# Performance work log

Measured on AMD Instinct MI355X. Metric: run time of the kernel, lower is better.

## Reference

```python
import jax, jax.numpy as jnp
import numpy as np

L, S, M, N, E, H = 1024, 1024, 256, 8, 512, 8


def embed_rotary(x, cos, sin):
    # x: [B, T, E]; interleaved rotate-half as in RotaryPositionEncoding.embed_rotary
    x2 = jnp.stack([-x[..., 1::2], x[..., 0::2]], axis=-1).reshape(x.shape)
    return x * cos + x2 * sin


def setup_inputs() -> dict:
    key = jax.random.key(0)
    ks = jax.random.split(key, 12)
    return {
        "query": jax.random.normal(ks[0], (L, N, E), jnp.float32),
        "key": jax.random.normal(ks[1], (S, N, E), jnp.float32),
        "value": jax.random.normal(ks[2], (S, N, E), jnp.float32),
        "in_proj_weight": jax.random.normal(ks[3], (3 * E, E), jnp.float32) / np.sqrt(E).astype(np.float32),
        "in_proj_bias": jnp.zeros((3 * E,), jnp.float32),
        "out_proj_weight": jax.random.normal(ks[4], (E, E), jnp.float32) / np.sqrt(E).astype(np.float32),
        "out_proj_bias": jnp.zeros((E,), jnp.float32),
        "rot_q": jax.random.normal(ks[5], (N, L, E, 2), jnp.float32),
        "rot_k": jax.random.normal(ks[6], (N, S, E, 2), jnp.float32),
        "k_mem": jax.random.normal(ks[7], (M, N, E), jnp.float32),
        "v_mem": jax.random.normal(ks[8], (M, N, E), jnp.float32),
        "gate_attn": jax.random.normal(ks[9], (H,), jnp.float32),
        "mem_mask": jax.random.randint(ks[10], (N, M), 0, 2).astype(bool),
        "num_heads": H,
    }


def reference(query, key, value, in_proj_weight, in_proj_bias, out_proj_weight,
              out_proj_bias, rot_q, rot_k, k_mem, v_mem, gate_attn, mem_mask, num_heads):
    L_, N_, E_ = query.shape
    S_ = key.shape[0]
    H_ = num_heads
    hd = E_ // H_
    scale = float(hd) ** -0.5
    # separate q/k/v projections (qkv not identical path)
    q = query @ in_proj_weight[:E_].T + in_proj_bias[:E_]
    k = key @ in_proj_weight[E_:2 * E_].T + in_proj_bias[E_:2 * E_]
    v = value @ in_proj_weight[2 * E_:].T + in_proj_bias[2 * E_:]
    q = q * scale
    # inline rotary PE (applied in batch-first layout, then back)
    q = embed_rotary(q.transpose(1, 0, 2), rot_q[..., 0], rot_q[..., 1]).transpose(1, 0, 2)
    k = embed_rotary(k.transpose(1, 0, 2), rot_k[..., 0], rot_k[..., 1]).transpose(1, 0, 2)
    qh = q.reshape(L_, N_, H_, hd).transpose(1, 2, 0, 3)  # [N,H,L,hd]
    kh = k.reshape(S_, N_, H_, hd).transpose(1, 2, 0, 3)  # [N,H,S,hd]
    vh = v.reshape(S_, N_, H_, hd).transpose(1, 2, 0, 3)
    scores = jnp.einsum('nhld,nhsd->nhls', qh, kh)
    # slot-competition: softmax over queries (slots), then renormalize over keys
    w = jax.nn.softmax(scores, axis=2) + 1e-8
    w = w / w.sum(axis=-1, keepdims=True)
    attn = jnp.einsum('nhls,nhsd->nhld', w, vh)
    # memorizing-transformer style memory K/V branch with sigmoid head gating
    Mm = k_mem.shape[0]
    km = k_mem.reshape(Mm, N_, H_, hd).transpose(1, 2, 0, 3)  # [N,H,M,hd]
    vm = v_mem.reshape(Mm, N_, H_, hd).transpose(1, 2, 0, 3)
    sm = jnp.einsum('nhld,nhmd->nhlm', qh, km)
    sm = jnp.where(mem_mask[:, None, None, :], -1e9, sm)  # additive -inf mask
    wm = jax.nn.softmax(sm, axis=-1)
    om = jnp.einsum('nhlm,nhmd->nhld', wm, vm)
    gate = jax.nn.sigmoid(gate_attn)[None, :, None, None]  # [1,H,1,1]
    attn = gate * om + (1.0 - gate) * attn
    out = attn.transpose(2, 0, 1, 3).reshape(L_, N_, E_)  # back to [L,N,E]
    return out @ out_proj_weight.T + out_proj_bias
```

## Files before the change

### kernel.cpp

```cpp
#include <hip/hip_runtime.h>
#include <hip/hip_bf16.h>

typedef __hip_bfloat16 bf16;
typedef __bf16 bf16x8 __attribute__((ext_vector_type(8)));
typedef float f32x4 __attribute__((ext_vector_type(4)));

#define LQ 1024
#define SK 1024
#define MMEM 256
#define NB 8
#define EE 512
#define NH 8
#define HD 64
#define NBH 64

__device__ inline __bf16 tobf(float f) {
  __hip_bfloat16 h = __float2bfloat16(f);
  return *reinterpret_cast<__bf16*>(&h);
}
__device__ inline float bf2f(__bf16 x) {
  unsigned short u; __builtin_memcpy(&u, &x, 2);
  unsigned int v = (unsigned int)u << 16;
  float f; __builtin_memcpy(&f, &v, 4);
  return f;
}
__device__ inline f32x4 MFMA(bf16x8 a, bf16x8 b, f32x4 c) {
  return __builtin_amdgcn_mfma_f32_16x16x32_bf16(a, b, c, 0, 0, 0);
}

__device__ inline bf16x8 load8(const float* p) {
  float4 a = *(const float4*)p;
  float4 b = *(const float4*)(p + 4);
  bf16x8 r;
  r[0] = tobf(a.x); r[1] = tobf(a.y); r[2] = tobf(a.z); r[3] = tobf(a.w);
  r[4] = tobf(b.x); r[5] = tobf(b.y); r[6] = tobf(b.z); r[7] = tobf(b.w);
  return r;
}

#define CVT_T0 524288
#define CVT_T3 98304
#define CVT_T4 32768
__global__ __launch_bounds__(256) void convert5(
    const float* __restrict__ q, const float* __restrict__ k,
    const float* __restrict__ v, const float* __restrict__ w,
    const float* __restrict__ o, bf16* __restrict__ qc, bf16* __restrict__ kc,
    bf16* __restrict__ vc, bf16* __restrict__ wc, bf16* __restrict__ oc)
{
  long long t = (long long)blockIdx.x * 256 + threadIdx.x;
  const float* src; bf16* dst; long long idx;
  if (t < CVT_T0)               { src = q; dst = qc; idx = t; }
  else if (t < 2 * CVT_T0)      { src = k; dst = kc; idx = t - CVT_T0; }
  else if (t < 3 * CVT_T0)      { src = v; dst = vc; idx = t - 2 * CVT_T0; }
  else if (t < 3 * CVT_T0 + CVT_T3) { src = w; dst = wc; idx = t - 3 * CVT_T0; }
  else                          { src = o; dst = oc; idx = t - 3 * CVT_T0 - CVT_T3; }
  *(bf16x8*)(dst + idx * 8) = load8(src + idx * 8);
}

__global__ __launch_bounds__(256) void gemm_proj3(
    const bf16* __restrict__ qc, const bf16* __restrict__ kc,
    const bf16* __restrict__ vc, const bf16* __restrict__ ipwb,
    const float* __restrict__ ipb, const float* __restrict__ rot_q,
    const float* __restrict__ rot_k, bf16* __restrict__ Qh,
    bf16* __restrict__ Kh, bf16* __restrict__ v_raw)
{
  __shared__ __align__(16) char smem[25600];
  __bf16 (*As)[40] = (__bf16(*)[40])smem;
  __bf16 (*Bs)[40] = (__bf16(*)[40])(smem + 5120);
  __bf16 (*Cs)[72] = (__bf16(*)[72])smem;
  const int z = blockIdx.z;
  const bf16* A = (z == 0) ? qc : (z == 1) ? kc : vc;
  const bf16* W = ipwb + (long long)z * EE * EE;
  const float* bias = ipb + z * EE;
  const float alpha = (z == 0) ? 0.125f : 1.f;
  const int tm0 = blockIdx.y << 6, tn0 = blockIdx.x << 8;
  const int t = threadIdx.x;
  const int lrow = t >> 2, lk = (t & 3) << 3;
  const int wave = t >> 6, lane = t & 63;
  const int wm = (wave & 1) << 5, wn = (wave >> 1) << 5;
  const int m16 = lane & 15, quad = lane >> 4;

  const f32x4 zero = {0.f, 0.f, 0.f, 0.f};
  f32x4 acc[4][2][2];
#pragma unroll
  for (int g = 0; g < 4; ++g)
#pragma unroll
    for (int mi = 0; mi < 2; ++mi)
#pragma unroll
      for (int ni = 0; ni < 2; ++ni) acc[g][mi][ni] = zero;

  const bf16* ag = A + (long long)(tm0 + lrow) * EE + lk;
  const bf16* bg = W + (long long)(tn0 + lrow) * EE + lk;
  for (int k0 = 0; k0 < EE; k0 += 32) {
    *(bf16x8*)&As[lrow][lk] = *(const bf16x8*)(ag + k0);
#pragma unroll
    for (int i = 0; i < 4; ++i)
      *(bf16x8*)&Bs[(i << 6) + lrow][lk] =
          *(const bf16x8*)(bg + (long long)(i << 6) * EE + k0);
    __syncthreads();
    bf16x8 a0 = *(bf16x8*)&As[wm + m16][quad << 3];
    bf16x8 a1 = *(bf16x8*)&As[wm + 16 + m16][quad << 3];
#pragma unroll
    for (int g = 0; g < 4; ++g) {
      bf16x8 b0 = *(bf16x8*)&Bs[(g << 6) + wn + m16][quad << 3];
      bf16x8 b1 = *(bf16x8*)&Bs[(g << 6) + wn + 16 + m16][quad << 3];
      acc[g][0][0] = MFMA(a0, b0, acc[g][0][0]);
      acc[g][0][1] = MFMA(a0, b1, acc[g][0][1]);
      acc[g][1][0] = MFMA(a1, b0, acc[g][1][0]);
      acc[g][1][1] = MFMA(a1, b1, acc[g][1][1]);
    }
    __syncthreads();
  }

  const int crow = t >> 2, ccol = (t & 3) << 4;
#pragma unroll
  for (int g = 0; g < 4; ++g) {
    __syncthreads();
    for (int mi = 0; mi < 2; ++mi)
      for (int ni = 0; ni < 2; ++ni) {
        int col = wn + (ni << 4) + m16;
        float bv = bias[tn0 + (g << 6) + col];
        for (int r = 0; r < 4; ++r)
          Cs[wm + (mi << 4) + (quad << 2) + r][col] =
              tobf((acc[g][mi][ni][r] + bv) * alpha);
      }
    __syncthreads();
    if (z == 2) {
      uint4 u0 = *(uint4*)&Cs[crow][ccol];
      uint4 u1 = *(uint4*)&Cs[crow][ccol + 8];
      long long gb = (long long)(tm0 + crow) * EE + tn0 + (g << 6) + ccol;
      *(uint4*)(v_raw + gb) = u0;
      *(uint4*)(v_raw + gb + 8) = u1;
    } else {
      const float* rot = (z == 0) ? rot_q : rot_k;
      bf16* Out = (z == 0) ? Qh : Kh;
      int grow = tm0 + crow;
      int l = grow >> 3, n = grow & 7;
      int e0 = tn0 + (g << 6) + ccol;
      int h = e0 >> 6, d0 = e0 & 63;
      const float* rp = rot + ((((long long)n * LQ + l) * EE + e0) << 1);
      __bf16 vals[16];
#pragma unroll
      for (int j = 0; j < 16; j += 2) {
        float4 cs4 = *(const float4*)(rp + (j << 1));
        float x0 = bf2f(Cs[crow][ccol + j]);
        float x1 = bf2f(Cs[crow][ccol + j + 1]);
        vals[j]     = tobf(x0 * cs4.x - x1 * cs4.y);
        vals[j + 1] = tobf(x1 * cs4.z + x0 * cs4.w);
      }
      bf16* dst = Out + ((((long long)(n * NH + h) * LQ) + l) * HD + d0);
      *(uint4*)dst = *(uint4*)&vals[0];
      *(uint4*)(dst + 8) = *(uint4*)&vals[8];
    }
  }
}

__global__ __launch_bounds__(256) void colsum_kernel(
    const bf16* __restrict__ Qh, const bf16* __restrict__ Kh,
    float* __restrict__ csum)
{
  __shared__ __align__(16) __bf16 Ks[64][72];
  __shared__ __align__(16) __bf16 Qs[64][72];
  __shared__ float cpart[64][2];
  const int b = blockIdx.y;
  const int st0 = blockIdx.x << 6;
  const int t = threadIdx.x;
  const int lrow = t >> 2, lcol = (t & 3) << 4;
  const int wave = t >> 6, lane = t & 63;
  const int wm = (wave & 1) << 5, wn = (wave >> 1) << 5;
  const int m16 = lane & 15, quad = lane >> 4;

  {
    const bf16* kp = Kh + ((long long)b * SK + st0 + lrow) * HD + lcol;
    *(bf16x8*)&Ks[lrow][lcol] = *(const bf16x8*)kp;
    *(bf16x8*)&Ks[lrow][lcol + 8] = *(const bf16x8*)(kp + 8);
  }
  __syncthreads();
  bf16x8 bk[2][2];
#pragma unroll
  for (int ni = 0; ni < 2; ++ni)
#pragma unroll
    for (int kh = 0; kh < 2; ++kh)
      bk[ni][kh] = *(bf16x8*)&Ks[wn + (ni << 4) + m16][(kh << 5) + (quad << 3)];
  __syncthreads();

  const f32x4 zero = {0.f, 0.f, 0.f, 0.f};
  float colp[2] = {0.f, 0.f};
  for (int lt = 0; lt < 16; ++lt) {
    const bf16* qp = Qh + ((long long)b * LQ + (lt << 6) + lrow) * HD + lcol;
    *(bf16x8*)&Qs[lrow][lcol] = *(const bf16x8*)qp;
    *(bf16x8*)&Qs[lrow][lcol + 8] = *(const bf16x8*)(qp + 8);
    __syncthreads();
    f32x4 s00 = zero, s01 = zero, s10 = zero, s11 = zero;
#pragma unroll
    for (int kh = 0; kh < 2; ++kh) {
      bf16x8 a0 = *(bf16x8*)&Qs[wm + m16][(kh << 5) + (quad << 3)];
      bf16x8 a1 = *(bf16x8*)&Qs[wm + 16 + m16][(kh << 5) + (quad << 3)];
      s00 = MFMA(a0, bk[0][kh], s00);
      s01 = MFMA(a0, bk[1][kh], s01);
      s10 = MFMA(a1, bk[0][kh], s10);
      s11 = MFMA(a1, bk[1][kh], s11);
    }
    f32x4 sacc[2][2] = {{s00, s01}, {s10, s11}};
#pragma unroll
    for (int mi = 0; mi < 2; ++mi)
#pragma unroll
      for (int ni = 0; ni < 2; ++ni)
#pragma unroll
        for (int r = 0; r < 4; ++r)
          colp[ni] += __expf(sacc[mi][ni][r]);
    __syncthreads();
  }
  for (int ni = 0; ni < 2; ++ni) {
    float v = colp[ni];
    v += __shfl_down(v, 32, 64);
    v += __shfl_down(v, 16, 64);
    if (quad == 0) cpart[wn + (ni << 4) + m16][wm >> 5] = v;
  }
  __syncthreads();
  if (t < 64) csum[b * SK + st0 + t] = cpart[t][0] + cpart[t][1];
}

__global__ __launch_bounds__(256) void vsum_kernel(
    const bf16* __restrict__ Vt, float* __restrict__ Vsum)
{
  int wid = blockIdx.x * 4 + (threadIdx.x >> 6);
  int lane = threadIdx.x & 63;
  const bf16* p = Vt + (long long)wid * SK + lane * 16;
  float s = 0.f;
  bf16x8 v0 = *(const bf16x8*)p;
  bf16x8 v1 = *(const bf16x8*)(p + 8);
#pragma unroll
  for (int j = 0; j < 8; ++j) s += bf2f(v0[j]) + bf2f(v1[j]);
  for (int off = 32; off; off >>= 1) s += __shfl_down(s, off, 64);
  if (lane == 0) Vsum[wid] = s;
}

__global__ __launch_bounds__(256) void attn_flash(
    const bf16* __restrict__ Qh, const bf16* __restrict__ Kh,
    const bf16* __restrict__ Vt, const float* __restrict__ csum,
    const float* __restrict__ Vsum, bf16* __restrict__ attn)
{
  __shared__ __align__(16) __bf16 Ks[64][72];
  __shared__ __align__(16) __bf16 Vs[64][72];
  __shared__ __align__(16) __bf16 Ps[64][72];
  __shared__ float rcs[SK];
  __shared__ float rpart[64][2];
  const int b = blockIdx.y;
  const int tm0 = blockIdx.x << 6;
  const int t = threadIdx.x;
  const int lrow = t >> 2, lcol = (t & 3) << 4;
  const int wave = t >> 6, lane = t & 63;
  const int wm = (wave & 1) << 5, wn = (wave >> 1) << 5;
  const int m16 = lane & 15, quad = lane >> 4;

#pragma unroll
  for (int i = 0; i < 4; ++i)
    rcs[t + i * 256] = 1.f / csum[b * SK + t + i * 256];
  {
    const bf16* qp = Qh + ((long long)b * LQ + tm0 + lrow) * HD + lcol;
    *(bf16x8*)&Ks[lrow][lcol] = *(const bf16x8*)qp;
    *(bf16x8*)&Ks[lrow][lcol + 8] = *(const bf16x8*)(qp + 8);
  }
  __syncthreads();
  bf16x8 aq[2][2];
#pragma unroll
  for (int mi = 0; mi < 2; ++mi)
#pragma unroll
    for (int kh = 0; kh < 2; ++kh)
      aq[mi][kh] = *(bf16x8*)&Ks[wm + (mi << 4) + m16][(kh << 5) + (quad << 3)];
  __syncthreads();

  const f32x4 zero = {0.f, 0.f, 0.f, 0.f};
  f32x4 o00 = zero, o01 = zero, o10 = zero, o11 = zero;
  float rsumr[2][4] = {{0.f, 0.f, 0.f, 0.f}, {0.f, 0.f, 0.f, 0.f}};

  for (int st = 0; st < 16; ++st) {
    const bf16* kp = Kh + ((long long)b * SK + (st << 6) + lrow) * HD + lcol;
    *(bf16x8*)&Ks[lrow][lcol] = *(const bf16x8*)kp;
    *(bf16x8*)&Ks[lrow][lcol + 8] = *(const bf16x8*)(kp + 8);
    const bf16* vp = Vt + ((long long)b * HD + lrow) * SK + (st << 6) + lcol;
    *(bf16x8*)&Vs[lrow][lcol] = *(const bf16x8*)vp;
    *(bf16x8*)&Vs[lrow][lcol + 8] = *(const bf16x8*)(vp + 8);
    __syncthreads();
    f32x4 s00 = zero, s01 = zero, s10 = zero, s11 = zero;
#pragma unroll
    for (int kh = 0; kh < 2; ++kh) {
      bf16x8 b0 = *(bf16x8*)&Ks[wn + m16][(kh << 5) + (quad << 3)];
      bf16x8 b1 = *(bf16x8*)&Ks[wn + 16 + m16][(kh << 5) + (quad << 3)];
      s00 = MFMA(aq[0][kh], b0, s00);
      s01 = MFMA(aq[0][kh], b1, s01);
      s10 = MFMA(aq[1][kh], b0, s10);
      s11 = MFMA(aq[1][kh], b1, s11);
    }
    f32x4 sacc[2][2] = {{s00, s01}, {s10, s11}};
#pragma unroll
    for (int mi = 0; mi < 2; ++mi)
#pragma unroll
      for (int ni = 0; ni < 2; ++ni) {
        int col = wn + (ni << 4) + m16;
        float rc = rcs[(st << 6) + col];
#pragma unroll
        for (int r = 0; r < 4; ++r) {
          float p = __expf(sacc[mi][ni][r]) * rc;
          rsumr[mi][r] += p;
          Ps[wm + (mi << 4) + (quad << 2) + r][col] = tobf(p);
        }
      }
    __syncthreads();
#pragma unroll
    for (int kh = 0; kh < 2; ++kh) {
      bf16x8 ap0 = *(bf16x8*)&Ps[wm + m16][(kh << 5) + (quad << 3)];
      bf16x8 ap1 = *(bf16x8*)&Ps[wm + 16 + m16][(kh << 5) + (quad << 3)];
      bf16x8 bv0 = *(bf16x8*)&Vs[wn + m16][(kh << 5) + (quad << 3)];
      bf16x8 bv1 = *(bf16x8*)&Vs[wn + 16 + m16][(kh << 5) + (quad << 3)];
      o00 = MFMA(ap0, bv0, o00);
      o01 = MFMA(ap0, bv1, o01);
      o10 = MFMA(ap1, bv0, o10);
      o11 = MFMA(ap1, bv1, o11);
    }
    __syncthreads();
  }
#pragma unroll
  for (int mi = 0; mi < 2; ++mi)
#pragma unroll
    for (int r = 0; r < 4; ++r) {
      float v = rsumr[mi][r];
      v += __shfl_xor(v, 1, 64);
      v += __shfl_xor(v, 2, 64);
      v += __shfl_xor(v, 4, 64);
      v += __shfl_xor(v, 8, 64);
      if (m16 == 0) rpart[wm + (mi << 4) + (quad << 2) + r][wn >> 5] = v;
    }
  __syncthreads();
  const float* vs = Vsum + b * HD;
  f32x4 oacc[2][2] = {{o00, o01}, {o10, o11}};
  for (int mi = 0; mi < 2; ++mi)
    for (int ni = 0; ni < 2; ++ni) {
      int col = wn + (ni << 4) + m16;
      float vsc = 1e-8f * vs[col];
      for (int r = 0; r < 4; ++r) {
        int row = wm + (mi << 4) + (quad << 2) + r;
        float rs = rpart[row][0] + rpart[row][1];
        Ps[row][col] = tobf((oacc[mi][ni][r] + vsc) / (rs + (float)SK * 1e-8f));
      }
    }
  __syncthreads();
  uint4 u0 = *(uint4*)&Ps[lrow][lcol];
  uint4 u1 = *(uint4*)&Ps[lrow][lcol + 8];
  long long gb = ((long long)b * LQ + tm0 + lrow) * HD + lcol;
  *(uint4*)(attn + gb) = u0;
  *(uint4*)(attn + gb + 8) = u1;
}

__global__ __launch_bounds__(256) void mem_flash(
    const bf16* __restrict__ Qh, const bf16* __restrict__ km,
    const bf16* __restrict__ vmt, const int* __restrict__ mask,
    bf16* __restrict__ omb)
{
  __shared__ __align__(16) __bf16 Ks[64][72];
  __shared__ __align__(16) __bf16 Vs[64][72];
  __shared__ __align__(16) __bf16 Ps[64][72];
  __shared__ float mskf[MMEM];
  __shared__ float rpart[64][2];
  const int b = blockIdx.y;
  const int n = b >> 3;
  const int tm0 = blockIdx.x << 6;
  const int t = threadIdx.x;
  const int wave = t >> 6, lane = t & 63;
  const int wm = (wave & 1) << 5, wn = (wave >> 1) << 5;
  const int m16 = lane & 15, quad = lane >> 4;
  const int lrow = t >> 2, lcol = (t & 3) << 4;

  mskf[t] = mask[n * MMEM + t] ? 0.f : 1.f;
  {
    const bf16* qp = Qh + ((long long)b * LQ + tm0 + lrow) * HD + lcol;
    *(bf16x8*)&Ks[lrow][lcol] = *(const bf16x8*)qp;
    *(bf16x8*)&Ks[lrow][lcol + 8] = *(const bf16x8*)(qp + 8);
  }
  __syncthreads();
  bf16x8 aq[2][2];
#pragma unroll
  for (int mi = 0; mi < 2; ++mi)
#pragma unroll
    for (int kh = 0; kh < 2; ++kh)
      aq[mi][kh] = *(bf16x8*)&Ks[wm + (mi << 4) + m16][(kh << 5) + (quad << 3)];
  __syncthreads();

  const f32x4 zero = {0.f, 0.f, 0.f, 0.f};
  f32x4 o00 = zero, o01 = zero, o10 = zero, o11 = zero;
  float rsumr[2][4] = {{0.f, 0.f, 0.f, 0.f}, {0.f, 0.f, 0.f, 0.f}};

  for (int mt = 0; mt < 4; ++mt) {
    const bf16* kp = km + ((long long)b * MMEM + (mt << 6) + lrow) * HD + lcol;
    *(bf16x8*)&Ks[lrow][lcol] = *(const bf16x8*)kp;
    *(bf16x8*)&Ks[lrow][lcol + 8] = *(const bf16x8*)(kp + 8);
    const bf16* vp = vmt + ((long long)b * HD + lrow) * MMEM + (mt << 6) + lcol;
    *(bf16x8*)&Vs[lrow][lcol] = *(const bf16x8*)vp;
    *(bf16x8*)&Vs[lrow][lcol + 8] = *(const bf16x8*)(vp + 8);
    __syncthreads();
    f32x4 s00 = zero, s01 = zero, s10 = zero, s11 = zero;
#pragma unroll
    for (int kh = 0; kh < 2; ++kh) {
      bf16x8 b0 = *(bf16x8*)&Ks[wn + m16][(kh << 5) + (quad << 3)];
      bf16x8 b1 = *(bf16x8*)&Ks[wn + 16 + m16][(kh << 5) + (quad << 3)];
      s00 = MFMA(aq[0][kh], b0, s00);
      s01 = MFMA(aq[0][kh], b1, s01);
      s10 = MFMA(aq[1][kh], b0, s10);
      s11 = MFMA(aq[1][kh], b1, s11);
    }
    f32x4 sacc[2][2] = {{s00, s01}, {s10, s11}};
#pragma unroll
    for (int mi = 0; mi < 2; ++mi)
#pragma unroll
      for (int ni = 0; ni < 2; ++ni) {
        int col = wn + (ni << 4) + m16;
        float mf = mskf[(mt << 6) + col];
#pragma unroll
        for (int r = 0; r < 4; ++r) {
          float p = __expf(sacc[mi][ni][r]) * mf;
          rsumr[mi][r] += p;
          Ps[wm + (mi << 4) + (quad << 2) + r][col] = tobf(p);
        }
      }
    __syncthreads();
#pragma unroll
    for (int kh = 0; kh < 2; ++kh) {
      bf16x8 ap0 = *(bf16x8*)&Ps[wm + m16][(kh << 5) + (quad << 3)];
      bf16x8 ap1 = *(bf16x8*)&Ps[wm + 16 + m16][(kh << 5) + (quad << 3)];
      bf16x8 bv0 = *(bf16x8*)&Vs[wn + m16][(kh << 5) + (quad << 3)];
      bf16x8 bv1 = *(bf16x8*)&Vs[wn + 16 + m16][(kh << 5) + (quad << 3)];
      o00 = MFMA(ap0, bv0, o00);
      o01 = MFMA(ap0, bv1, o01);
      o10 = MFMA(ap1, bv0, o10);
      o11 = MFMA(ap1, bv1, o11);
    }
    __syncthreads();
  }
#pragma unroll
  for (int mi = 0; mi < 2; ++mi)
#pragma unroll
    for (int r = 0; r < 4; ++r) {
      float v = rsumr[mi][r];
      v += __shfl_xor(v, 1, 64);
      v += __shfl_xor(v, 2, 64);
      v += __shfl_xor(v, 4, 64);
      v += __shfl_xor(v, 8, 64);
      if (m16 == 0) rpart[wm + (mi << 4) + (quad << 2) + r][wn >> 5] = v;
    }
  __syncthreads();
  f32x4 oacc[2][2] = {{o00, o01}, {o10, o11}};
  for (int mi = 0; mi < 2; ++mi)
    for (int ni = 0; ni < 2; ++ni) {
      int col = wn + (ni << 4) + m16;
      for (int r = 0; r < 4; ++r) {
        int row = wm + (mi << 4) + (quad << 2) + r;
        float rs = rpart[row][0] + rpart[row][1];
        Ps[row][col] = tobf(oacc[mi][ni][r] / rs);
      }
    }
  __syncthreads();
  uint4 u0 = *(uint4*)&Ps[lrow][lcol];
  uint4 u1 = *(uint4*)&Ps[lrow][lcol + 8];
  long long gb = ((long long)b * LQ + tm0 + lrow) * HD + lcol;
  *(uint4*)(omb + gb) = u0;
  *(uint4*)(omb + gb + 8) = u1;
}

__global__ __launch_bounds__(256) void gemm_out(
    const bf16* __restrict__ attn, const bf16* __restrict__ omb,
    const float* __restrict__ gate, const bf16* __restrict__ opwb,
    const float* __restrict__ opb, float* __restrict__ out)
{
  __shared__ __align__(16) __bf16 As[64][40];
  __shared__ __align__(16) __bf16 Bs[64][40];
  __shared__ float sg[NH];
  const int tm0 = blockIdx.y << 6, tn0 = blockIdx.x << 6;
  const int t = threadIdx.x;
  const int lrow = t >> 2, lk = (t & 3) << 3;
  const int wave = t >> 6, lane = t & 63;
  const int wm = (wave & 1) << 5, wn = (wave >> 1) << 5;
  const int m16 = lane & 15, quad = lane >> 4;

  if (t < NH) sg[t] = 1.f / (1.f + __expf(-gate[t]));
  __syncthreads();

  const f32x4 zero = {0.f, 0.f, 0.f, 0.f};
  f32x4 acc00 = zero, acc01 = zero, acc10 = zero, acc11 = zero;

  const int row = tm0 + lrow;
  const int l = row >> 3, n = row & 7;
  const bf16* bg = opwb + (long long)(tn0 + lrow) * EE + lk;
  for (int k0 = 0; k0 < EE; k0 += 32) {
    int e = k0 + lk;
    int h = e >> 6, d = e & 63;
    float g = sg[h];
    long long src = (((long long)(n * NH + h) * LQ) + l) * HD + d;
    bf16x8 a8 = *(const bf16x8*)(attn + src);
    bf16x8 o8 = *(const bf16x8*)(omb + src);
    bf16x8 ap;
#pragma unroll
    for (int j = 0; j < 8; ++j)
      ap[j] = tobf(g * bf2f(o8[j]) + (1.f - g) * bf2f(a8[j]));
    *(bf16x8*)&As[lrow][lk] = ap;
    *(bf16x8*)&Bs[lrow][lk] = *(const bf16x8*)(bg + k0);
    __syncthreads();
    bf16x8 a0 = *(bf16x8*)&As[wm + m16][quad << 3];
    bf16x8 a1 = *(bf16x8*)&As[wm + 16 + m16][quad << 3];
    bf16x8 b0 = *(bf16x8*)&Bs[wn + m16][quad << 3];
    bf16x8 b1 = *(bf16x8*)&Bs[wn + 16 + m16][quad << 3];
    acc00 = MFMA(a0, b0, acc00);
    acc01 = MFMA(a0, b1, acc01);
    acc10 = MFMA(a1, b0, acc10);
    acc11 = MFMA(a1, b1, acc11);
    __syncthreads();
  }
  f32x4 accs[2][2] = {{acc00, acc01}, {acc10, acc11}};
  for (int mi = 0; mi < 2; ++mi)
    for (int ni = 0; ni < 2; ++ni) {
      int col = tn0 + wn + (ni << 4) + m16;
      float bv = opb[col];
      long long base = (long long)(tm0 + wm + (mi << 4) + (quad << 2)) * EE + col;
      for (int r = 0; r < 4; ++r)
        out[base + (long long)r * EE] = accs[mi][ni][r] + bv;
    }
}

__global__ __launch_bounds__(256) void v_transpose(
    const bf16* __restrict__ raw, bf16* __restrict__ Vt)
{
  long long i = (long long)blockIdx.x * 256 + threadIdx.x;
  int e = (int)(i & 511);
  long long t2 = i >> 9;
  int n = (int)(t2 & 7);
  int s = (int)(t2 >> 3);
  int h = e >> 6, d = e & 63;
  Vt[(((long long)(n * NH + h) * HD) + d) * SK + s] = raw[i];
}

__global__ __launch_bounds__(256) void mem_prep(
    const float* __restrict__ k_mem, const float* __restrict__ v_mem,
    bf16* __restrict__ km, bf16* __restrict__ vmt)
{
  long long i = (long long)blockIdx.x * 256 + threadIdx.x;
  int e = (int)(i & 511);
  long long t2 = i >> 9;
  int n = (int)(t2 & 7);
  int m = (int)(t2 >> 3);
  int h = e >> 6, d = e & 63;
  km[(((long long)(n * NH + h) * MMEM) + m) * HD + d] = (bf16)k_mem[i];
  vmt[(((long long)(n * NH + h) * HD) + d) * MMEM + m] = (bf16)v_mem[i];
}

extern "C" void kernel_launch(void* const* d_in, const int* in_sizes, int n_in,
                              void* d_out, int out_size, void* d_ws, size_t ws_size,
                              hipStream_t stream) {
  const float* query = (const float*)d_in[0];
  const float* key   = (const float*)d_in[1];
  const float* value = (const float*)d_in[2];
  const float* ipw   = (const float*)d_in[3];
  const float* ipb   = (const float*)d_in[4];
  const float* opw   = (const float*)d_in[5];
  const float* opb   = (const float*)d_in[6];
  const float* rot_q = (const float*)d_in[7];
  const float* rot_k = (const float*)d_in[8];
  const float* k_mem = (const float*)d_in[9];
  const float* v_mem = (const float*)d_in[10];
  const float* gate  = (const float*)d_in[11];
  const int*  mask   = (const int*)d_in[12];
  float* out = (float*)d_out;

  char* w = (char*)d_ws;
  size_t off = 0;
  auto carve = [&](size_t bytes) -> char* {
    char* p = w + off;
    off += (bytes + 255) & ~(size_t)255;
    return p;
  };
  bf16* qc    = (bf16*)carve((size_t)LQ * NB * EE * 2);
  bf16* kc    = (bf16*)carve((size_t)SK * NB * EE * 2);
  bf16* vc    = (bf16*)carve((size_t)SK * NB * EE * 2);
  bf16* ipwb  = (bf16*)carve((size_t)3 * EE * EE * 2);
  bf16* opwb  = (bf16*)carve((size_t)EE * EE * 2);
  bf16* v_raw = (bf16*)carve((size_t)SK * NB * EE * 2);
  bf16* Qh    = (bf16*)carve((size_t)NBH * LQ * HD * 2);
  bf16* Kh    = (bf16*)carve((size_t)NBH * SK * HD * 2);
  bf16* Vt    = (bf16*)carve((size_t)NBH * HD * SK * 2);
  bf16* km    = (bf16*)carve((size_t)NBH * MMEM * HD * 2);
  bf16* vmt   = (bf16*)carve((size_t)NBH * HD * MMEM * 2);
  float* csum = (float*)carve((size_t)NBH * SK * 4);
  float* Vsum = (float*)carve((size_t)NBH * HD * 4);
  bf16* attn  = (bf16*)carve((size_t)NBH * LQ * HD * 2);
  bf16* omb   = (bf16*)carve((size_t)NBH * LQ * HD * 2);
  if (off > ws_size) {
    hipMemsetAsync(d_out, 0, (size_t)out_size * 4, stream);
    return;
  }

  convert5<<<(3 * CVT_T0 + CVT_T3 + CVT_T4) / 256, 256, 0, stream>>>(
      query, key, value, ipw, opw, qc, kc, vc, ipwb, opwb);

  gemm_proj3<<<dim3(EE / 256, (LQ * NB) / 64, 3), 256, 0, stream>>>(
      qc, kc, vc, ipwb, ipb, rot_q, rot_k, Qh, Kh, v_raw);

  v_transpose<<<(SK * NB * EE) / 256, 256, 0, stream>>>(v_raw, Vt);
  vsum_kernel<<<(NBH * HD) / 4, 256, 0, stream>>>(Vt, Vsum);
  mem_prep<<<(MMEM * NB * EE) / 256, 256, 0, stream>>>(k_mem, v_mem, km, vmt);

  colsum_kernel<<<dim3(SK / 64, NBH), 256, 0, stream>>>(Qh, Kh, csum);

  attn_flash<<<dim3(LQ / 64, NBH), 256, 0, stream>>>(Qh, Kh, Vt, csum, Vsum, attn);
  mem_flash<<<dim3(LQ / 64, NBH), 256, 0, stream>>>(Qh, km, vmt, mask, omb);

  gemm_out<<<dim3(EE / 64, (LQ * NB) / 64, 1), 256, 0, stream>>>(attn, omb, gate, opwb, opb, out);
}
```

Before: 350.6 us.

## Retile projection GEMM to 128x128 with direct global-to-LDS loads

Reworks the QKV projection GEMM from 64x256 tiles with K-step 32 to 128x128 tiles with K-step 64, giving each wave a 64x64 sub-tile with 4x4 MFMA accumulators. Operand tiles are loaded with global_load_lds straight into unpadded shared memory, skipping the register round-trip. The epilogue is restructured to stage the whole tile in LDS once and write it out in a single pass with rotary applied. The goal is more MFMA work per byte loaded and fewer barriers. In exchange it uses more registers and LDS, and the unpadded LDS layout may cause bank conflicts.

```diff
diff --git a/kernel.cpp b/kernel.cpp
--- a/kernel.cpp
+++ b/kernel.cpp
@@ -28,6 +28,12 @@
   return __builtin_amdgcn_mfma_f32_16x16x32_bf16(a, b, c, 0, 0, 0);
 }
 
+__device__ inline void gload_lds16(const bf16* g, void* l) {
+  __builtin_amdgcn_global_load_lds(
+      (const __attribute__((address_space(1))) void*)g,
+      (__attribute__((address_space(3))) void*)l, 16, 0, 0);
+}
+
 __device__ inline bf16x8 load8(const float* p) {
   float4 a = *(const float4*)p;
   float4 b = *(const float4*)(p + 4);
@@ -63,91 +69,99 @@
     const float* __restrict__ rot_k, bf16* __restrict__ Qh,
     bf16* __restrict__ Kh, bf16* __restrict__ v_raw)
 {
-  __shared__ __align__(16) char smem[25600];
-  __bf16 (*As)[40] = (__bf16(*)[40])smem;
-  __bf16 (*Bs)[40] = (__bf16(*)[40])(smem + 5120);
-  __bf16 (*Cs)[72] = (__bf16(*)[72])smem;
+  __shared__ __align__(16) char smem[33792];
+  __bf16* As = (__bf16*)smem;
+  __bf16* Bs = (__bf16*)(smem + 16384);
   const int z = blockIdx.z;
   const bf16* A = (z == 0) ? qc : (z == 1) ? kc : vc;
   const bf16* W = ipwb + (long long)z * EE * EE;
   const float* bias = ipb + z * EE;
   const float alpha = (z == 0) ? 0.125f : 1.f;
-  const int tm0 = blockIdx.y << 6, tn0 = blockIdx.x << 8;
+  const int tm0 = blockIdx.y << 7, tn0 = blockIdx.x << 7;
   const int t = threadIdx.x;
-  const int lrow = t >> 2, lk = (t & 3) << 3;
   const int wave = t >> 6, lane = t & 63;
-  const int wm = (wave & 1) << 5, wn = (wave >> 1) << 5;
+  const int wrow0 = (wave & 1) << 6, wcol0 = (wave >> 1) << 6;
   const int m16 = lane & 15, quad = lane >> 4;
 
   const f32x4 zero = {0.f, 0.f, 0.f, 0.f};
-  f32x4 acc[4][2][2];
-#pragma unroll
-  for (int g = 0; g < 4; ++g)
-#pragma unroll
-    for (int mi = 0; mi < 2; ++mi)
-#pragma unroll
-      for (int ni = 0; ni < 2; ++ni) acc[g][mi][ni] = zero;
-
-  const bf16* ag = A + (long long)(tm0 + lrow) * EE + lk;
-  const bf16* bg = W + (long long)(tn0 + lrow) * EE + lk;
-  for (int k0 = 0; k0 < EE; k0 += 32) {
-    *(bf16x8*)&As[lrow][lk] = *(const bf16x8*)(ag + k0);
-#pragma unroll
-    for (int i = 0; i < 4; ++i)
-      *(bf16x8*)&Bs[(i << 6) + lrow][lk] =
-          *(const bf16x8*)(bg + (long long)(i << 6) * EE + k0);
-    __syncthreads();
-    bf16x8 a0 = *(bf16x8*)&As[wm + m16][quad << 3];
-    bf16x8 a1 = *(bf16x8*)&As[wm + 16 + m16][quad << 3];
-#pragma unroll
-    for (int g = 0; g < 4; ++g) {
-      bf16x8 b0 = *(bf16x8*)&Bs[(g << 6) + wn + m16][quad << 3];
-      bf16x8 b1 = *(bf16x8*)&Bs[(g << 6) + wn + 16 + m16][quad << 3];
-      acc[g][0][0] = MFMA(a0, b0, acc[g][0][0]);
-      acc[g][0][1] = MFMA(a0, b1, acc[g][0][1]);
-      acc[g][1][0] = MFMA(a1, b0, acc[g][1][0]);
-      acc[g][1][1] = MFMA(a1, b1, acc[g][1][1]);
-    }
-    __syncthreads();
-  }
-
-  const int crow = t >> 2, ccol = (t & 3) << 4;
-#pragma unroll
-  for (int g = 0; g < 4; ++g) {
-    __syncthreads();
-    for (int mi = 0; mi < 2; ++mi)
-      for (int ni = 0; ni < 2; ++ni) {
-        int col = wn + (ni << 4) + m16;
-        float bv = bias[tn0 + (g << 6) + col];
-        for (int r = 0; r < 4; ++r)
-          Cs[wm + (mi << 4) + (quad << 2) + r][col] =
-              tobf((acc[g][mi][ni][r] + bv) * alpha);
+  f32x4 acc[4][4];
+#pragma unroll
+  for (int mi = 0; mi < 4; ++mi)
+#pragma unroll
+    for (int ni = 0; ni < 4; ++ni) acc[mi][ni] = zero;
+
+  const bf16* Ab = A + (long long)tm0 * EE;
+  const bf16* Bb = W + (long long)tn0 * EE;
+  const int ob_u = wave << 10;
+
+  for (int k0 = 0; k0 < EE; k0 += 64) {
+#pragma unroll
+    for (int c = 0; c < 4; ++c) {
+      int ob = (c << 12) + ob_u;
+      int obl = ob + (lane << 4);
+      int row = obl >> 7;
+      int ce = (obl & 127) >> 1;
+      gload_lds16(Ab + (long long)row * EE + k0 + ce, smem + ob);
+      gload_lds16(Bb + (long long)row * EE + k0 + ce, smem + 16384 + ob);
+    }
+    __syncthreads();
+#pragma unroll
+    for (int kh = 0; kh < 2; ++kh) {
+      bf16x8 av[4], bv[4];
+#pragma unroll
+      for (int i = 0; i < 4; ++i) {
+        av[i] = *(bf16x8*)(As + ((wrow0 + (i << 4) + m16) << 6) + (kh << 5) + (quad << 3));
+        bv[i] = *(bf16x8*)(Bs + ((wcol0 + (i << 4) + m16) << 6) + (kh << 5) + (quad << 3));
       }
-    __syncthreads();
-    if (z == 2) {
-      uint4 u0 = *(uint4*)&Cs[crow][ccol];
-      uint4 u1 = *(uint4*)&Cs[crow][ccol + 8];
-      long long gb = (long long)(tm0 + crow) * EE + tn0 + (g << 6) + ccol;
-      *(uint4*)(v_raw + gb) = u0;
-      *(uint4*)(v_raw + gb + 8) = u1;
-    } else {
-      const float* rot = (z == 0) ? rot_q : rot_k;
-      bf16* Out = (z == 0) ? Qh : Kh;
-      int grow = tm0 + crow;
-      int l = grow >> 3, n = grow & 7;
-      int e0 = tn0 + (g << 6) + ccol;
+#pragma unroll
+      for (int mi = 0; mi < 4; ++mi)
+#pragma unroll
+        for (int ni = 0; ni < 4; ++ni)
+          acc[mi][ni] = MFMA(av[mi], bv[ni], acc[mi][ni]);
+    }
+    __syncthreads();
+  }
+
+  __bf16 (*Cs)[132] = (__bf16(*)[132])smem;
+#pragma unroll
+  for (int mi = 0; mi < 4; ++mi)
+#pragma unroll
+    for (int ni = 0; ni < 4; ++ni) {
+      int col = wcol0 + (ni << 4) + m16;
+      float bv = bias[tn0 + col];
+#pragma unroll
+      for (int r = 0; r < 4; ++r)
+        Cs[wrow0 + (mi << 4) + (quad << 2) + r][col] =
+            tobf((acc[mi][ni][r] + bv) * alpha);
+    }
+  __syncthreads();
+
+  const int crow = t >> 1, ch0 = (t & 1) << 6;
+  const int grow = tm0 + crow;
+  if (z == 2) {
+    long long gb = (long long)grow * EE + tn0 + ch0;
+#pragma unroll
+    for (int j = 0; j < 64; j += 8)
+      *(uint4*)(v_raw + gb + j) = *(uint4*)&Cs[crow][ch0 + j];
+  } else {
+    const int l = grow >> 3, n = grow & 7;
+    const float* rot = (z == 0) ? rot_q : rot_k;
+    bf16* Out2 = (z == 0) ? Qh : Kh;
+#pragma unroll
+    for (int cc = 0; cc < 4; ++cc) {
+      int e0 = tn0 + ch0 + (cc << 4);
       int h = e0 >> 6, d0 = e0 & 63;
       const float* rp = rot + ((((long long)n * LQ + l) * EE + e0) << 1);
       __bf16 vals[16];
 #pragma unroll
       for (int j = 0; j < 16; j += 2) {
         float4 cs4 = *(const float4*)(rp + (j << 1));
-        float x0 = bf2f(Cs[crow][ccol + j]);
-        float x1 = bf2f(Cs[crow][ccol + j + 1]);
+        float x0 = bf2f(Cs[crow][ch0 + (cc << 4) + j]);
+        float x1 = bf2f(Cs[crow][ch0 + (cc << 4) + j + 1]);
         vals[j]     = tobf(x0 * cs4.x - x1 * cs4.y);
         vals[j + 1] = tobf(x1 * cs4.z + x0 * cs4.w);
       }
-      bf16* dst = Out + ((((long long)(n * NH + h) * LQ) + l) * HD + d0);
+      bf16* dst = Out2 + ((((long long)(n * NH + h) * LQ) + l) * HD + d0);
       *(uint4*)dst = *(uint4*)&vals[0];
       *(uint4*)(dst + 8) = *(uint4*)&vals[8];
     }
@@ -599,7 +613,7 @@
   convert5<<<(3 * CVT_T0 + CVT_T3 + CVT_T4) / 256, 256, 0, stream>>>(
       query, key, value, ipw, opw, qc, kc, vc, ipwb, opwb);
 
-  gemm_proj3<<<dim3(EE / 256, (LQ * NB) / 64, 3), 256, 0, stream>>>(
+  gemm_proj3<<<dim3(EE / 128, (LQ * NB) / 128, 3), 256, 0, stream>>>(
       qc, kc, vc, ipwb, ipb, rot_q, rot_k, Qh, Kh, v_raw);
 
   v_transpose<<<(SK * NB * EE) / 256, 256, 0, stream>>>(v_raw, Vt);
```

Result: no change. 354.7 us (+1.2%).
